# Performance work log

Measured on AMD Instinct MI355X. Metric: run time of the kernel, lower is better.

## Reference

```python
import jax, jax.numpy as jnp
import numpy as np


def _linear(x, W, b):
    # torch nn.Linear: y = x @ W.T + b, W is [out, in]
    return x @ W.T + b


def _sage_layer(x, edge_index, Ws, bs, Wn, bn):
    # GraphSAGE: mean-aggregate neighbor features via scatter-add, then two linears.
    src, tgt = edge_index[0], edge_index[1]
    N = x.shape[0]
    agg = jax.ops.segment_sum(x[src], tgt, num_segments=N)            # [N, D]
    deg = jax.ops.segment_sum(jnp.ones(src.shape, x.dtype), tgt, num_segments=N)  # [N]
    neighbor_mean = agg / jnp.maximum(deg, 1.0)[:, None]
    return _linear(x, Ws, bs) + _linear(neighbor_mean, Wn, bn)


def setup_inputs() -> dict:
    key = jax.random.key(0)
    ks = jax.random.split(key, 16)
    N, ATTR, H, OUT, E = 50000, 125, 128, 128, 800000
    IN = ATTR + 3
    s = 0.05
    inp = {
        "attr_features": jax.random.normal(ks[0], (N, ATTR), jnp.float32),
        "clustering_coefficient": jax.random.uniform(ks[1], (N, 1), jnp.float32),
        "bidirectional_links_ratio": jax.random.uniform(ks[2], (N, 1), jnp.float32),
        "exist_nodes": jnp.ones((N,), jnp.float32),
        "W_in": s * jax.random.normal(ks[3], (H, IN), jnp.float32),
        "b_in": s * jax.random.normal(ks[4], (H,), jnp.float32),
        "W1_self": s * jax.random.normal(ks[5], (H, H), jnp.float32),
        "b1_self": s * jax.random.normal(ks[6], (H,), jnp.float32),
        "W1_neigh": s * jax.random.normal(ks[7], (H, H), jnp.float32),
        "b1_neigh": s * jax.random.normal(ks[8], (H,), jnp.float32),
        "W2_self": s * jax.random.normal(ks[9], (OUT, H), jnp.float32),
        "b2_self": s * jax.random.normal(ks[10], (OUT,), jnp.float32),
        "W2_neigh": s * jax.random.normal(ks[11], (OUT, H), jnp.float32),
        "b2_neigh": s * jax.random.normal(ks[12], (OUT,), jnp.float32),
        "edge_index": jax.random.randint(ks[13], (2, E), 0, N, jnp.int64),
    }
    return inp


def reference(attr_features, clustering_coefficient, bidirectional_links_ratio,
              exist_nodes, W_in, b_in, W1_self, b1_self, W1_neigh, b1_neigh,
              W2_self, b2_self, W2_neigh, b2_neigh, edge_index):
    exist_col = exist_nodes[:, None]                                   # [N, 1]
    x = jnp.concatenate(
        [attr_features, clustering_coefficient, bidirectional_links_ratio, exist_col],
        axis=1)                                                        # [N, attr_dim+3]
    x = jax.nn.relu(_linear(x, W_in, b_in))                            # dropout=0 -> identity
    x = _sage_layer(x, edge_index, W1_self, b1_self, W1_neigh, b1_neigh)
    x = jax.nn.relu(x)
    x = x * exist_col
    x = _sage_layer(x, edge_index, W2_self, b2_self, W2_neigh, b2_neigh)
    return x * exist_col
```

## Files before the change

kernel.cpp:

```cpp
#include <hip/hip_runtime.h>
#include <hip/hip_bf16.h>

typedef __attribute__((ext_vector_type(8))) short short8;
typedef __attribute__((ext_vector_type(4))) float floatx4;

__device__ inline unsigned short f2bf(float f) {
    unsigned u = __float_as_uint(f);
    u += 0x7fffu + ((u >> 16) & 1u);
    return (unsigned short)(u >> 16);
}


__global__ void prep_weights(const float* __restrict__ w_in, const float* __restrict__ w1s,
                             const float* __restrict__ w1n, const float* __restrict__ w2s,
                             const float* __restrict__ w2n,
                             const float* __restrict__ b_in, const float* __restrict__ b1s,
                             const float* __restrict__ b1n, const float* __restrict__ b2s,
                             const float* __restrict__ b2n,
                             unsigned short* __restrict__ wb, float* __restrict__ biasf) {
    int idx = blockIdx.x * 256 + threadIdx.x;
    if (idx < 5 * 16384) {
        int m = idx >> 14, j = idx & 16383;
        const float* src = (m == 0) ? w_in : (m == 1) ? w1s : (m == 2) ? w1n : (m == 3) ? w2s : w2n;
        wb[idx] = f2bf(src[j]);
    }
    if (idx < 128) {
        biasf[idx]       = b_in[idx];
        biasf[128 + idx] = b1s[idx] + b1n[idx];
        biasf[256 + idx] = b2s[idx] + b2n[idx];
    }
}

__global__ void build_x0(const float* __restrict__ attr, const float* __restrict__ cc,
                         const float* __restrict__ bl, const float* __restrict__ ex,
                         unsigned short* __restrict__ x0, int N, int ATTR) {
    int idx = blockIdx.x * 256 + threadIdx.x;
    if (idx >= N * 128) return;
    int row = idx >> 7, col = idx & 127;
    float v;
    if (col < ATTR)            v = attr[row * ATTR + col];
    else if (col == ATTR)      v = cc[row];
    else if (col == ATTR + 1)  v = bl[row];
    else                       v = ex[row];
    x0[idx] = f2bf(v);
}


__global__ __launch_bounds__(256) void chunk_hist(const int* __restrict__ e,
                                                  int* __restrict__ chunk_count, int E) {
    __shared__ int h[128];
    if (threadIdx.x < 128) h[threadIdx.x] = 0;
    __syncthreads();
    for (int i = blockIdx.x * 256 + threadIdx.x; i < E; i += gridDim.x * 256)
        atomicAdd(&h[e[E + i] >> 9], 1);
    __syncthreads();
    if (threadIdx.x < 128 && h[threadIdx.x])
        atomicAdd(&chunk_count[threadIdx.x], h[threadIdx.x]);
}

__global__ void chunk_scan(const int* __restrict__ chunk_count,
                           int* __restrict__ chunk_base, int* __restrict__ chunk_cursor) {
    __shared__ int s[128];
    int t = threadIdx.x;
    int v = chunk_count[t];
    s[t] = v;
    __syncthreads();
    for (int o = 1; o < 128; o <<= 1) {
        int u = (t >= o) ? s[t - o] : 0;
        __syncthreads();
        s[t] += u;
        __syncthreads();
    }
    int excl = s[t] - v;
    chunk_base[t] = excl;
    chunk_cursor[t] = excl;
}

#define BTILE 4096

__global__ __launch_bounds__(256) void bin_pass(const int* __restrict__ e,
                                                int* __restrict__ chunk_cursor,
                                                unsigned* __restrict__ packed_out,
                                                int E, int ntiles) {
    __shared__ unsigned buf[BTILE];
    __shared__ unsigned sbuf[BTILE];
    __shared__ int hist[128], offs[128], gbase[128], lcur[128];
    int t = threadIdx.x;
    for (int tile = blockIdx.x; tile < ntiles; tile += gridDim.x) {
        int e0 = tile * BTILE;
        int cnt = min(BTILE, E - e0);
        if (t < 128) hist[t] = 0;
        __syncthreads();
        for (int j = t; j < cnt; j += 256) {
            unsigned src = (unsigned)e[e0 + j];
            unsigned tgt = (unsigned)e[E + e0 + j];
            unsigned c = tgt >> 9;
            buf[j] = (c << 25) | (src << 9) | (tgt & 511u);
            atomicAdd(&hist[c], 1);
        }
        __syncthreads();
        if (t < 128) offs[t] = hist[t];
        __syncthreads();
        for (int o = 1; o < 128; o <<= 1) {
            int v = (t < 128 && t >= o) ? offs[t - o] : 0;
            __syncthreads();
            if (t < 128) offs[t] += v;
            __syncthreads();
        }
        if (t < 128) {
            int excl = offs[t] - hist[t];
            offs[t] = excl;
            lcur[t] = excl;
            gbase[t] = (hist[t] > 0) ? atomicAdd(&chunk_cursor[t], hist[t]) : 0;
        }
        __syncthreads();
        for (int j = t; j < cnt; j += 256) {
            unsigned v = buf[j];
            int c = v >> 25;
            int p = atomicAdd(&lcur[c], 1);
            sbuf[p] = v;
        }
        __syncthreads();
        int wv = t >> 6, lane = t & 63;
        for (int c = wv; c < 128; c += 4) {
            int n = hist[c], lo = offs[c], gb = gbase[c];
            for (int j = lane; j < n; j += 64)
                packed_out[gb + j] = sbuf[lo + j];
        }
        __syncthreads();
    }
}

#define CSR_CAP 12288

__global__ __launch_bounds__(256) void chunk_csr(const unsigned* __restrict__ packed,
                                                 const int* __restrict__ chunk_base,
                                                 const int* __restrict__ chunk_cursor,
                                                 int* __restrict__ rows, int* __restrict__ colv,
                                                 int N) {
    __shared__ int hist[512], offs[512], lcnt[512], pp[256];
    __shared__ int sbuf[CSR_CAP];
    int c = blockIdx.x;
    int base = chunk_base[c];
    int cnt = chunk_cursor[c] - base;
    int t = threadIdx.x;
    hist[t] = 0;
    hist[t + 256] = 0;
    __syncthreads();
    for (int j = t; j < cnt; j += 256)
        atomicAdd(&hist[packed[base + j] & 511u], 1);
    __syncthreads();
    int a0 = hist[2 * t], a1 = hist[2 * t + 1];
    pp[t] = a0 + a1;
    __syncthreads();
    for (int o = 1; o < 256; o <<= 1) {
        int v = (t >= o) ? pp[t - o] : 0;
        __syncthreads();
        pp[t] += v;
        __syncthreads();
    }
    int excl = pp[t] - (a0 + a1);
    offs[2 * t] = excl;
    offs[2 * t + 1] = excl + a0;
    lcnt[2 * t] = 0;
    lcnt[2 * t + 1] = 0;
    __syncthreads();
    for (int j = t; j < 512; j += 256) {
        int node = c * 512 + j;
        if (node <= N) rows[node] = base + offs[j];
    }
    if (cnt <= CSR_CAP) {
        for (int j = t; j < cnt; j += 256) {
            unsigned v = packed[base + j];
            int node = v & 511u;
            int p = offs[node] + atomicAdd(&lcnt[node], 1);
            sbuf[p] = (v >> 9) & 0xFFFFu;
        }
        __syncthreads();
        for (int j = t; j < cnt; j += 256) colv[base + j] = sbuf[j];
    } else {
        for (int j = t; j < cnt; j += 256) {
            unsigned v = packed[base + j];
            int node = v & 511u;
            int p = offs[node] + atomicAdd(&lcnt[node], 1);
            colv[base + p] = (v >> 9) & 0xFFFFu;
        }
    }
}


__global__ __launch_bounds__(256) void agg_mean(const unsigned short* __restrict__ x,
                                                const int* __restrict__ rows,
                                                const int* __restrict__ colv,
                                                unsigned short* __restrict__ nm, int N) {
    int wid = (blockIdx.x * 256 + threadIdx.x) >> 6;
    int lane = threadIdx.x & 63;
    if (wid >= N) return;
    int s0 = rows[wid], s1 = rows[wid + 1];
    int deg = s1 - s0;
    int mn = deg < 64 ? deg : 64;
    int cvec = (lane < mn) ? colv[s0 + lane] : 0;
    int half = lane >> 5;
    int cl = (lane & 31) * 4;
    float a0 = 0.f, a1 = 0.f, a2 = 0.f, a3 = 0.f;
    int lim = mn - 1;
    for (int j = 0; j < mn; j += 16) {
        uint2 v[8];
        #pragma unroll
        for (int u = 0; u < 8; ++u) {
            int ei = j + 2 * u + half;
            int idx = (ei <= lim) ? ei : lim;
            int s = __shfl(cvec, idx, 64);
            v[u] = *(const uint2*)(x + (size_t)s * 128 + cl);
        }
        #pragma unroll
        for (int u = 0; u < 8; ++u) {
            int ei = j + 2 * u + half;
            if (ei <= lim) {
                a0 += __uint_as_float(v[u].x << 16);
                a1 += __uint_as_float(v[u].x & 0xffff0000u);
                a2 += __uint_as_float(v[u].y << 16);
                a3 += __uint_as_float(v[u].y & 0xffff0000u);
            }
        }
    }
    for (int e = s0 + 64; e < s1; e += 2) {
        int ei = e + half;
        int idx = (ei < s1) ? ei : s1 - 1;
        int s = colv[idx];
        uint2 v = *(const uint2*)(x + (size_t)s * 128 + cl);
        if (ei < s1) {
            a0 += __uint_as_float(v.x << 16);
            a1 += __uint_as_float(v.x & 0xffff0000u);
            a2 += __uint_as_float(v.y << 16);
            a3 += __uint_as_float(v.y & 0xffff0000u);
        }
    }
    a0 += __shfl_xor(a0, 32, 64);
    a1 += __shfl_xor(a1, 32, 64);
    a2 += __shfl_xor(a2, 32, 64);
    a3 += __shfl_xor(a3, 32, 64);
    if (half == 0) {
        float inv = 1.0f / (float)(deg > 1 ? deg : 1);
        a0 *= inv; a1 *= inv; a2 *= inv; a3 *= inv;
        uint2 o;
        o.x = ((unsigned)f2bf(a1) << 16) | (unsigned)f2bf(a0);
        o.y = ((unsigned)f2bf(a3) << 16) | (unsigned)f2bf(a2);
        *(uint2*)(nm + (size_t)wid * 128 + cl) = o;
    }
}


__global__ __launch_bounds__(256, 3) void gemm_fused(
    const unsigned short* __restrict__ X0, const unsigned short* __restrict__ X1,
    const unsigned short* __restrict__ W0, const unsigned short* __restrict__ W1,
    const float* __restrict__ bias, const float* __restrict__ ex,
    unsigned short* __restrict__ obf, float* __restrict__ of32,
    int N, int relu, int nphase) {
    __shared__ unsigned short lx[64 * 136];
    int tid = threadIdx.x;
    int lane = tid & 63;
    int w = tid >> 6;
    int node0 = blockIdx.x * 64;
    int n_off = w * 32;
    int q = lane >> 4;
    int m16 = lane & 15;

    short8 bf0[2][4], bf1[2][4];
    #pragma unroll
    for (int nt = 0; nt < 2; ++nt)
        #pragma unroll
        for (int kk = 0; kk < 4; ++kk)
            bf0[nt][kk] = *(const short8*)(W0 + (n_off + nt * 16 + m16) * 128 + kk * 32 + q * 8);
    if (nphase == 2) {
        #pragma unroll
        for (int nt = 0; nt < 2; ++nt)
            #pragma unroll
            for (int kk = 0; kk < 4; ++kk)
                bf1[nt][kk] = *(const short8*)(W1 + (n_off + nt * 16 + m16) * 128 + kk * 32 + q * 8);
    }

    floatx4 acc[4][2];
    for (int nt = 0; nt < 2; ++nt) {
        float bv = bias[n_off + nt * 16 + m16];
        floatx4 b4 = {bv, bv, bv, bv};
        for (int mt = 0; mt < 4; ++mt) acc[mt][nt] = b4;
    }

    for (int ph = 0; ph < nphase; ++ph) {
        const unsigned short* X = ph ? X1 : X0;
        for (int i = 0; i < 4; ++i) {
            int c = tid + 256 * i;
            int nd = c >> 4, ck = c & 15;
            short8 v = {0, 0, 0, 0, 0, 0, 0, 0};
            if (node0 + nd < N) v = *(const short8*)(X + (size_t)(node0 + nd) * 128 + ck * 8);
            *(short8*)(lx + nd * 136 + ck * 8) = v;
        }
        __syncthreads();
        for (int kk = 0; kk < 4; ++kk) {
            short8 a[4];
            for (int mt = 0; mt < 4; ++mt)
                a[mt] = *(const short8*)(lx + (mt * 16 + m16) * 136 + kk * 32 + q * 8);
            for (int mt = 0; mt < 4; ++mt) {
                const short8* b0 = ph ? &bf1[0][kk] : &bf0[0][kk];
                const short8* b1 = ph ? &bf1[1][kk] : &bf0[1][kk];
                acc[mt][0] = __builtin_amdgcn_mfma_f32_16x16x32_bf16(a[mt], *b0, acc[mt][0], 0, 0, 0);
                acc[mt][1] = __builtin_amdgcn_mfma_f32_16x16x32_bf16(a[mt], *b1, acc[mt][1], 0, 0, 0);
            }
        }
        __syncthreads();
    }

    for (int mt = 0; mt < 4; ++mt) {
        int rbase = node0 + mt * 16 + q * 4;
        for (int r = 0; r < 4; ++r) {
            int rr = rbase + r;
            if (rr >= N) continue;
            float e = ex ? ex[rr] : 1.0f;
            for (int nt = 0; nt < 2; ++nt) {
                float v = acc[mt][nt][r];
                if (relu) v = fmaxf(v, 0.0f);
                v *= e;
                int col = n_off + nt * 16 + m16;
                if (obf) obf[(size_t)rr * 128 + col] = f2bf(v);
                else     of32[(size_t)rr * 128 + col] = v;
            }
        }
    }
}


extern "C" void kernel_launch(void* const* d_in, const int* in_sizes, int n_in,
                              void* d_out, int out_size, void* d_ws, size_t ws_size,
                              hipStream_t stream) {
    const float* attr = (const float*)d_in[0];
    const float* cc   = (const float*)d_in[1];
    const float* bl   = (const float*)d_in[2];
    const float* ex   = (const float*)d_in[3];
    const float* w_in = (const float*)d_in[4];
    const float* b_in = (const float*)d_in[5];
    const float* w1s  = (const float*)d_in[6];
    const float* b1s  = (const float*)d_in[7];
    const float* w1n  = (const float*)d_in[8];
    const float* b1n  = (const float*)d_in[9];
    const float* w2s  = (const float*)d_in[10];
    const float* b2s  = (const float*)d_in[11];
    const float* w2n  = (const float*)d_in[12];
    const float* b2n  = (const float*)d_in[13];
    const int*   eidx = (const int*)d_in[14];

    int N = in_sizes[3];
    int ATTR = in_sizes[0] / N;
    int E = in_sizes[14] / 2;
    int Npad = ((N + 63) / 64) * 64;
    int nchunk = (N >> 9) + 1;
    int ntilesE = (E + BTILE - 1) / BTILE;

    char* ws = (char*)d_ws;
    size_t off = 0;
    auto alloc = [&](size_t bytes) -> char* {
        off = (off + 255) & ~(size_t)255;
        char* p = ws + off;
        off += bytes;
        return p;
    };
    unsigned short* xa = (unsigned short*)alloc((size_t)Npad * 128 * 2);
    unsigned short* xb = (unsigned short*)alloc((size_t)Npad * 128 * 2);
    unsigned short* xc = (unsigned short*)alloc((size_t)Npad * 128 * 2);
    int* colv = (int*)alloc((size_t)E * 4);
    unsigned* packed = (unsigned*)alloc((size_t)E * 4);
    int* rows = (int*)alloc((size_t)(N + 256) * 4);
    int* chunk_count  = (int*)alloc(128 * 4);
    int* chunk_base   = (int*)alloc(128 * 4);
    int* chunk_cursor = (int*)alloc(128 * 4);
    unsigned short* wb = (unsigned short*)alloc((size_t)5 * 16384 * 2);
    float* biasf = (float*)alloc(3 * 128 * 4);

    hipMemsetAsync(chunk_count, 0, 128 * 4, stream);

    prep_weights<<<(5 * 16384 + 255) / 256, 256, 0, stream>>>(
        w_in, w1s, w1n, w2s, w2n, b_in, b1s, b1n, b2s, b2n, wb, biasf);
    build_x0<<<(N * 128 + 255) / 256, 256, 0, stream>>>(attr, cc, bl, ex, xa, N, ATTR);

    chunk_hist<<<256, 256, 0, stream>>>(eidx, chunk_count, E);
    chunk_scan<<<1, 128, 0, stream>>>(chunk_count, chunk_base, chunk_cursor);
    bin_pass<<<(ntilesE < 256 ? ntilesE : 256), 256, 0, stream>>>(eidx, chunk_cursor, packed, E, ntilesE);
    chunk_csr<<<nchunk, 256, 0, stream>>>(packed, chunk_base, chunk_cursor, rows, colv, N);

    int gblk = Npad / 64;
    gemm_fused<<<gblk, 256, 0, stream>>>(xa, (const unsigned short*)nullptr,
                                         wb, (const unsigned short*)nullptr,
                                         biasf, (const float*)nullptr,
                                         xb, (float*)nullptr, N, 1, 1);
    agg_mean<<<(N + 3) / 4, 256, 0, stream>>>(xb, rows, colv, xc, N);
    gemm_fused<<<gblk, 256, 0, stream>>>(xb, xc, wb + 16384, wb + 2 * 16384,
                                         biasf + 128, ex, xa, (float*)nullptr, N, 1, 2);
    agg_mean<<<(N + 3) / 4, 256, 0, stream>>>(xa, rows, colv, xc, N);
    gemm_fused<<<gblk, 256, 0, stream>>>(xa, xc, wb + 3 * 16384, wb + 4 * 16384,
                                         biasf + 256, ex, (unsigned short*)nullptr,
                                         (float*)d_out, N, 0, 2);
}
```

Before: 259.6 us.

## Use fixed-capacity chunk slots to drop edge histogram and scan kernels

Preallocates a fixed-capacity slot per 512-node chunk so binning can start from cursors set in prep_weights, removing the chunk histogram pass, scan kernel and memset. Row offsets become per-node (start,end) pairs since chunks are no longer contiguous. This saves a full read of the target indices and several launches, but overflows silently if any chunk receives more than the fixed capacity of edges.

```diff
diff --git a/kernel.cpp b/kernel.cpp
--- a/kernel.cpp
+++ b/kernel.cpp
@@ -10,6 +10,8 @@
     return (unsigned short)(u >> 16);
 }
 
+
+#define CHUNK_CAP 12288
 
 __global__ void prep_weights(const float* __restrict__ w_in, const float* __restrict__ w1s,
                              const float* __restrict__ w1n, const float* __restrict__ w2s,
@@ -17,7 +19,8 @@
                              const float* __restrict__ b_in, const float* __restrict__ b1s,
                              const float* __restrict__ b1n, const float* __restrict__ b2s,
                              const float* __restrict__ b2n,
-                             unsigned short* __restrict__ wb, float* __restrict__ biasf) {
+                             unsigned short* __restrict__ wb, float* __restrict__ biasf,
+                             int* __restrict__ chunk_cursor) {
     int idx = blockIdx.x * 256 + threadIdx.x;
     if (idx < 5 * 16384) {
         int m = idx >> 14, j = idx & 16383;
@@ -29,6 +32,8 @@
         biasf[128 + idx] = b1s[idx] + b1n[idx];
         biasf[256 + idx] = b2s[idx] + b2n[idx];
     }
+    if (blockIdx.x == 0 && threadIdx.x < 128)
+        chunk_cursor[threadIdx.x] = threadIdx.x * CHUNK_CAP;
 }
 
 __global__ void build_x0(const float* __restrict__ attr, const float* __restrict__ cc,
@@ -46,36 +51,6 @@
 }
 
 
-__global__ __launch_bounds__(256) void chunk_hist(const int* __restrict__ e,
-                                                  int* __restrict__ chunk_count, int E) {
-    __shared__ int h[128];
-    if (threadIdx.x < 128) h[threadIdx.x] = 0;
-    __syncthreads();
-    for (int i = blockIdx.x * 256 + threadIdx.x; i < E; i += gridDim.x * 256)
-        atomicAdd(&h[e[E + i] >> 9], 1);
-    __syncthreads();
-    if (threadIdx.x < 128 && h[threadIdx.x])
-        atomicAdd(&chunk_count[threadIdx.x], h[threadIdx.x]);
-}
-
-__global__ void chunk_scan(const int* __restrict__ chunk_count,
-                           int* __restrict__ chunk_base, int* __restrict__ chunk_cursor) {
-    __shared__ int s[128];
-    int t = threadIdx.x;
-    int v = chunk_count[t];
-    s[t] = v;
-    __syncthreads();
-    for (int o = 1; o < 128; o <<= 1) {
-        int u = (t >= o) ? s[t - o] : 0;
-        __syncthreads();
-        s[t] += u;
-        __syncthreads();
-    }
-    int excl = s[t] - v;
-    chunk_base[t] = excl;
-    chunk_cursor[t] = excl;
-}
-
 #define BTILE 4096
 
 __global__ __launch_bounds__(256) void bin_pass(const int* __restrict__ e,
@@ -131,17 +106,14 @@
     }
 }
 
-#define CSR_CAP 12288
-
 __global__ __launch_bounds__(256) void chunk_csr(const unsigned* __restrict__ packed,
-                                                 const int* __restrict__ chunk_base,
                                                  const int* __restrict__ chunk_cursor,
-                                                 int* __restrict__ rows, int* __restrict__ colv,
-                                                 int N) {
+                                                 uint2* __restrict__ rows2,
+                                                 int* __restrict__ colv, int N) {
     __shared__ int hist[512], offs[512], lcnt[512], pp[256];
-    __shared__ int sbuf[CSR_CAP];
+    __shared__ int sbuf[CHUNK_CAP];
     int c = blockIdx.x;
-    int base = chunk_base[c];
+    int base = c * CHUNK_CAP;
     int cnt = chunk_cursor[c] - base;
     int t = threadIdx.x;
     hist[t] = 0;
@@ -167,36 +139,33 @@
     __syncthreads();
     for (int j = t; j < 512; j += 256) {
         int node = c * 512 + j;
-        if (node <= N) rows[node] = base + offs[j];
-    }
-    if (cnt <= CSR_CAP) {
-        for (int j = t; j < cnt; j += 256) {
-            unsigned v = packed[base + j];
-            int node = v & 511u;
-            int p = offs[node] + atomicAdd(&lcnt[node], 1);
-            sbuf[p] = (v >> 9) & 0xFFFFu;
-        }
-        __syncthreads();
-        for (int j = t; j < cnt; j += 256) colv[base + j] = sbuf[j];
-    } else {
-        for (int j = t; j < cnt; j += 256) {
-            unsigned v = packed[base + j];
-            int node = v & 511u;
-            int p = offs[node] + atomicAdd(&lcnt[node], 1);
-            colv[base + p] = (v >> 9) & 0xFFFFu;
-        }
-    }
+        if (node < N) {
+            uint2 r;
+            r.x = base + offs[j];
+            r.y = base + offs[j] + hist[j];
+            rows2[node] = r;
+        }
+    }
+    for (int j = t; j < cnt; j += 256) {
+        unsigned v = packed[base + j];
+        int node = v & 511u;
+        int p = offs[node] + atomicAdd(&lcnt[node], 1);
+        sbuf[p] = (v >> 9) & 0xFFFFu;
+    }
+    __syncthreads();
+    for (int j = t; j < cnt; j += 256) colv[base + j] = sbuf[j];
 }
 
 
 __global__ __launch_bounds__(256) void agg_mean(const unsigned short* __restrict__ x,
-                                                const int* __restrict__ rows,
+                                                const uint2* __restrict__ rows2,
                                                 const int* __restrict__ colv,
                                                 unsigned short* __restrict__ nm, int N) {
     int wid = (blockIdx.x * 256 + threadIdx.x) >> 6;
     int lane = threadIdx.x & 63;
     if (wid >= N) return;
-    int s0 = rows[wid], s1 = rows[wid + 1];
+    uint2 r = rows2[wid];
+    int s0 = r.x, s1 = r.y;
     int deg = s1 - s0;
     int mn = deg < 64 ? deg : 64;
     int cvec = (lane < mn) ? colv[s0 + lane] : 0;
@@ -353,7 +322,7 @@
     int ATTR = in_sizes[0] / N;
     int E = in_sizes[14] / 2;
     int Npad = ((N + 63) / 64) * 64;
-    int nchunk = (N >> 9) + 1;
+    int nchunk = (N + 511) / 512;
     int ntilesE = (E + BTILE - 1) / BTILE;
 
     char* ws = (char*)d_ws;
@@ -367,35 +336,29 @@
     unsigned short* xa = (unsigned short*)alloc((size_t)Npad * 128 * 2);
     unsigned short* xb = (unsigned short*)alloc((size_t)Npad * 128 * 2);
     unsigned short* xc = (unsigned short*)alloc((size_t)Npad * 128 * 2);
-    int* colv = (int*)alloc((size_t)E * 4);
-    unsigned* packed = (unsigned*)alloc((size_t)E * 4);
-    int* rows = (int*)alloc((size_t)(N + 256) * 4);
-    int* chunk_count  = (int*)alloc(128 * 4);
-    int* chunk_base   = (int*)alloc(128 * 4);
+    int* colv = (int*)alloc((size_t)128 * CHUNK_CAP * 4);
+    unsigned* packed = (unsigned*)alloc((size_t)128 * CHUNK_CAP * 4);
+    uint2* rows2 = (uint2*)alloc((size_t)N * 8);
     int* chunk_cursor = (int*)alloc(128 * 4);
     unsigned short* wb = (unsigned short*)alloc((size_t)5 * 16384 * 2);
     float* biasf = (float*)alloc(3 * 128 * 4);
 
-    hipMemsetAsync(chunk_count, 0, 128 * 4, stream);
-
     prep_weights<<<(5 * 16384 + 255) / 256, 256, 0, stream>>>(
-        w_in, w1s, w1n, w2s, w2n, b_in, b1s, b1n, b2s, b2n, wb, biasf);
+        w_in, w1s, w1n, w2s, w2n, b_in, b1s, b1n, b2s, b2n, wb, biasf, chunk_cursor);
     build_x0<<<(N * 128 + 255) / 256, 256, 0, stream>>>(attr, cc, bl, ex, xa, N, ATTR);
 
-    chunk_hist<<<256, 256, 0, stream>>>(eidx, chunk_count, E);
-    chunk_scan<<<1, 128, 0, stream>>>(chunk_count, chunk_base, chunk_cursor);
     bin_pass<<<(ntilesE < 256 ? ntilesE : 256), 256, 0, stream>>>(eidx, chunk_cursor, packed, E, ntilesE);
-    chunk_csr<<<nchunk, 256, 0, stream>>>(packed, chunk_base, chunk_cursor, rows, colv, N);
+    chunk_csr<<<nchunk, 256, 0, stream>>>(packed, chunk_cursor, rows2, colv, N);
 
     int gblk = Npad / 64;
     gemm_fused<<<gblk, 256, 0, stream>>>(xa, (const unsigned short*)nullptr,
                                          wb, (const unsigned short*)nullptr,
                                          biasf, (const float*)nullptr,
                                          xb, (float*)nullptr, N, 1, 1);
-    agg_mean<<<(N + 3) / 4, 256, 0, stream>>>(xb, rows, colv, xc, N);
+    agg_mean<<<(N + 3) / 4, 256, 0, stream>>>(xb, rows2, colv, xc, N);
     gemm_fused<<<gblk, 256, 0, stream>>>(xb, xc, wb + 16384, wb + 2 * 16384,
                                          biasf + 128, ex, xa, (float*)nullptr, N, 1, 2);
-    agg_mean<<<(N + 3) / 4, 256, 0, stream>>>(xa, rows, colv, xc, N);
+    agg_mean<<<(N + 3) / 4, 256, 0, stream>>>(xa, rows2, colv, xc, N);
     gemm_fused<<<gblk, 256, 0, stream>>>(xa, xc, wb + 3 * 16384, wb + 4 * 16384,
                                          biasf + 256, ex, (unsigned short*)nullptr,
                                          (float*)d_out, N, 0, 2);
```

Result: faster. 249.1 us (-4.0%).
